# Kernel optimization log

Hardware: AMD Instinct MI355X
Metric: run time of the kernel (lower is better)

The kernel has to match this reference:

```python
import jax, jax.numpy as jnp
import numpy as np

D_MODEL = 1024
N_HEAD = 16


def setup_inputs() -> dict:
    key = jax.random.key(0)
    kx, kw = jax.random.split(key)
    x = jax.random.normal(kx, (4, 2048, D_MODEL), dtype=jnp.float32)
    # fused QKV projection weight, torch Linear: y = x @ W.T, W: [3*d_model, d_model]
    W_qkv = jax.random.normal(kw, (3 * D_MODEL, D_MODEL), dtype=jnp.float32) * (D_MODEL ** -0.5)
    return {"x": x, "W_qkv": W_qkv}


def reference(x, W_qkv):
    B, T, C = x.shape
    hd = C // N_HEAD
    qkv = jnp.einsum('btc,fc->btf', x, W_qkv)  # [B,T,3C]
    q, k, v = jnp.split(qkv, 3, axis=-1)
    # [B, H, T, hd]
    q = q.reshape(B, T, N_HEAD, hd).transpose(0, 2, 1, 3)
    k = k.reshape(B, T, N_HEAD, hd).transpose(0, 2, 1, 3)
    v = v.reshape(B, T, N_HEAD, hd).transpose(0, 2, 1, 3)
    scale = 1.0 / jnp.sqrt(jnp.asarray(hd, dtype=x.dtype))
    scores = jnp.einsum('bhqd,bhkd->bhqk', q, k) * scale  # [B,H,T,T]
    causal = jnp.tril(jnp.ones((T, T), dtype=bool))
    scores = jnp.where(causal, scores, jnp.asarray(-jnp.inf, dtype=scores.dtype))
    w = jax.nn.softmax(scores, axis=-1)
    out = jnp.einsum('bhqk,bhkd->bhqd', w, v)  # [B,H,T,hd]
    return out
```

## Files before the change

### kernel.cpp

```cpp
#include <hip/hip_runtime.h>
#include <hip/hip_bf16.h>
#include <math.h>

#define D_MODEL 1024
#define N_HEAD  16
#define HD      64
#define B_SZ    4
#define T_SEQ   2048
#define M_TOT   (B_SZ * T_SEQ)
#define N_TOT   (3 * D_MODEL)

typedef __bf16 bf16_t;
typedef __bf16 bf16x8 __attribute__((ext_vector_type(8)));
typedef __bf16 bf16x4 __attribute__((ext_vector_type(4)));
typedef __bf16 bf16x2 __attribute__((ext_vector_type(2)));
typedef float  f32x4  __attribute__((ext_vector_type(4)));
typedef float  f32x16 __attribute__((ext_vector_type(16)));
typedef int    i32x4  __attribute__((ext_vector_type(4)));

#define Q_PRESCALE 0.18033688011112042f

__device__ inline float fexp2(float x) { return __builtin_amdgcn_exp2f(x); }

__global__ __launch_bounds__(256) void cvt_f32_bf16(const float* __restrict__ in,
                                                    bf16_t* __restrict__ out, int n4) {
  int i = blockIdx.x * blockDim.x + threadIdx.x;
  int stride = gridDim.x * blockDim.x;
  for (; i < n4; i += stride) {
    float4 v = ((const float4*)in)[i];
    bf16x4 o;
    o[0] = (bf16_t)v.x; o[1] = (bf16_t)v.y; o[2] = (bf16_t)v.z; o[3] = (bf16_t)v.w;
    ((bf16x4*)out)[i] = o;
  }
}

__global__ __launch_bounds__(256) void qkv_gemm(const bf16_t* __restrict__ xb,
                                                const bf16_t* __restrict__ wb,
                                                bf16_t* __restrict__ Q,
                                                bf16_t* __restrict__ Kf,
                                                bf16_t* __restrict__ Vf) {
  __shared__ alignas(16) bf16_t smem[24576];
  bf16_t* a_lds = smem;
  bf16_t* b_lds = smem + 12288;
  bf16_t* c_lds = smem;

  const int tid  = threadIdx.x;
  const int wave = tid >> 6;
  const int lane = tid & 63;
  const int bm = blockIdx.y * 128;
  const int bn = blockIdx.x * 128;
  const int sec = bn >> 10;

  f32x4 acc[4][4] = {};

  const int sRow  = lane >> 2;
  const int sCol8 = (lane & 3) ^ ((lane >> 3) & 3);
  const int fr = lane & 15;
  const int fk = lane >> 4;
  const int wm = (wave >> 1) * 64;
  const int wn = (wave & 1) * 64;

  auto stage = [&](int buf, int kk) {
#pragma unroll
    for (int c = 0; c < 2; ++c) {
      const int chunk = wave * 2 + c;
      const bf16_t* gA = &xb[(size_t)(bm + chunk * 16 + sRow) * D_MODEL + kk + sCol8 * 8];
      __builtin_amdgcn_global_load_lds(
          (__attribute__((address_space(1))) void*)(void*)gA,
          (__attribute__((address_space(3))) void*)&a_lds[buf * 4096 + chunk * 512], 16, 0, 0);
      const bf16_t* gB = &wb[(size_t)(bn + chunk * 16 + sRow) * D_MODEL + kk + sCol8 * 8];
      __builtin_amdgcn_global_load_lds(
          (__attribute__((address_space(1))) void*)(void*)gB,
          (__attribute__((address_space(3))) void*)&b_lds[buf * 4096 + chunk * 512], 16, 0, 0);
    }
  };

  auto loadFrags = [&](int buf, bf16x8 af[4], bf16x8 bfr[4]) {
#pragma unroll
    for (int mt = 0; mt < 4; ++mt) {
      const int row = wm + mt * 16 + fr;
      af[mt] = *(const bf16x8*)&a_lds[buf * 4096 + row * 32 + (fk ^ ((fr >> 1) & 3)) * 8];
    }
#pragma unroll
    for (int nt = 0; nt < 4; ++nt) {
      const int row = wn + nt * 16 + fr;
      bfr[nt] = *(const bf16x8*)&b_lds[buf * 4096 + row * 32 + (fk ^ ((fr >> 1) & 3)) * 8];
    }
  };

  auto mfmaAll = [&](bf16x8 af[4], bf16x8 bfr[4]) {
    __builtin_amdgcn_s_setprio(1);
#pragma unroll
    for (int mt = 0; mt < 4; ++mt)
#pragma unroll
      for (int nt = 0; nt < 4; ++nt)
        acc[mt][nt] = __builtin_amdgcn_mfma_f32_16x16x32_bf16(af[mt], bfr[nt], acc[mt][nt], 0, 0, 0);
    __builtin_amdgcn_s_setprio(0);
  };

  stage(0, 0);
  stage(1, 32);
  int cur = 0;
  for (int t = 0; t < 31; ++t) {
    asm volatile("s_waitcnt vmcnt(4)" ::: "memory");
    __builtin_amdgcn_s_barrier();
    __builtin_amdgcn_sched_barrier(0);
    bf16x8 af[4], bfr[4];
    loadFrags(cur, af, bfr);
    if (t < 30) stage((t + 2) % 3, (t + 2) * 32);
    mfmaAll(af, bfr);
    cur = (cur + 1) % 3;
  }
  asm volatile("s_waitcnt vmcnt(0)" ::: "memory");
  __builtin_amdgcn_s_barrier();
  __builtin_amdgcn_sched_barrier(0);
  {
    bf16x8 af[4], bfr[4];
    loadFrags(cur, af, bfr);
    mfmaAll(af, bfr);
  }

  const int cRowBase = (lane >> 4) * 4;
  const int cCol     = lane & 15;

  if (sec == 2) {
#pragma unroll
    for (int mt = 0; mt < 4; ++mt) {
#pragma unroll
      for (int nt = 0; nt < 4; ++nt) {
        const int hn = (bn & 1023) + wn + nt * 16 + cCol;
        const int h  = hn >> 6;
        const int d  = hn & 63;
        const int mbase = bm + wm + mt * 16 + cRowBase;
        const int b  = mbase >> 11;
        const int t0 = mbase & 2047;
        const int kvt = t0 >> 5, tt0 = t0 & 31;
        const int idx = (d >> 5) * 2 + (tt0 >> 4);
        const int h2  = (tt0 >> 3) & 1;
        const int j0  = tt0 & 7;
        bf16x4 pk;
        pk[0] = (bf16_t)acc[mt][nt][0]; pk[1] = (bf16_t)acc[mt][nt][1];
        pk[2] = (bf16_t)acc[mt][nt][2]; pk[3] = (bf16_t)acc[mt][nt][3];
        const size_t bhOff = (size_t)(b * N_HEAD + h) * (T_SEQ * HD);
        *(bf16x4*)&Vf[bhOff + (size_t)(((kvt * 4 + idx) * 64 + h2 * 32 + (d & 31)) * 8 + j0)] = pk;
      }
    }
  } else {
    __syncthreads();
    const float qs = (sec == 0) ? Q_PRESCALE : 1.0f;
#pragma unroll
    for (int mt = 0; mt < 4; ++mt)
#pragma unroll
      for (int nt = 0; nt < 4; ++nt)
#pragma unroll
        for (int r = 0; r < 4; ++r) {
          const int mloc = wm + mt * 16 + cRowBase + r;
          const int nloc = wn + nt * 16 + cCol;
          c_lds[mloc * 132 + nloc] = (bf16_t)(acc[mt][nt][r] * qs);
        }
    __syncthreads();

    const int row = tid >> 1;
    const int nh  = tid & 1;
    const int m = bm + row;
    const int b = m >> 11, t = m & 2047;
    const int h = ((bn & 1023) + nh * 64) >> 6;
    const size_t bhOff = (size_t)(b * N_HEAD + h) * (T_SEQ * HD);

    if (sec == 0) {
      bf16_t* qp = Q + bhOff + (size_t)t * HD;
#pragma unroll
      for (int o = 0; o < 16; ++o) {
        bf16x4 vv = *(const bf16x4*)&c_lds[row * 132 + nh * 64 + o * 4];
        *(bf16x4*)&qp[o * 4] = vv;
      }
    } else {
      const int kvt = t >> 5, lk = t & 31;
#pragma unroll
      for (int o = 0; o < 16; ++o) {
        const int d0 = o * 4;
        const int cc = d0 >> 4, h2 = (d0 >> 3) & 1, j0 = d0 & 7;
        bf16x4 vv = *(const bf16x4*)&c_lds[row * 132 + nh * 64 + d0];
        *(bf16x4*)&Kf[bhOff + (size_t)(((kvt * 4 + cc) * 64 + h2 * 32 + lk) * 8 + j0)] = vv;
      }
    }
  }
}

__device__ inline int pack_bf16(float lo, float hi) {
  bf16x2 v; v[0] = (bf16_t)lo; v[1] = (bf16_t)hi;
  return __builtin_bit_cast(int, v);
}
__device__ inline void permswap(int& a, int& b) {
  asm volatile("v_permlane32_swap_b32 %0, %1" : "+v"(a), "+v"(b));
}

__global__ __launch_bounds__(256, 4) void attn_fwd(const bf16_t* __restrict__ Q,
                                                   const bf16_t* __restrict__ Kf,
                                                   const bf16_t* __restrict__ Vf,
                                                   float* __restrict__ out) {
  __shared__ float o_sh[2][64][33];
  __shared__ float m_sh[2][32];
  __shared__ float l_sh[2][32];

  const int tid  = threadIdx.x;
  const int wave = tid >> 6;
  const int lane = tid & 63;
  const int l31  = lane & 31;
  const int hi   = lane >> 5;

  const int f   = blockIdx.x;
  const int bh  = ((f & 7) << 3) | ((f >> 3) & 7);
  const int pr  = f >> 6;
  const int grp = wave >> 1;
  const int isWriter = wave & 1;
  const int chunk = grp ? (63 - pr) : pr;
  const int q0 = chunk * 32;
  const int n  = chunk + 1;
  const int h  = (n + 1) >> 1;
  const int j0 = isWriter ? h : 0;
  const int j1 = isWriter ? n : h;

  const bf16_t* Qp = Q  + (size_t)bh * T_SEQ * HD;
  const bf16_t* Kp = Kf + (size_t)bh * T_SEQ * HD;
  const bf16_t* Vp = Vf + (size_t)bh * T_SEQ * HD;
  float* op = out + (size_t)bh * T_SEQ * HD;

  bf16x8 qf[4];
#pragma unroll
  for (int c = 0; c < 4; ++c)
    qf[c] = *(const bf16x8*)&Qp[(size_t)(q0 + l31) * HD + c * 16 + hi * 8];

  f32x16 o0 = {}, o1 = {};
  float m_run = -INFINITY;
  float l_run = 0.f;

  if (j0 < j1) {
    const bf16_t* kp = Kp + (size_t)j0 * 2048 + lane * 8;
    const bf16_t* vp = Vp + (size_t)j0 * 2048 + lane * 8;
    bf16x8 kA[4], vA[4];
#pragma unroll
    for (int c = 0; c < 4; ++c) kA[c] = *(const bf16x8*)(kp + c * 512);
    kp += 2048;

    for (int j = j0; j < j1; ++j) {
      const int kv0 = j * 32;
#pragma unroll
      for (int idx = 0; idx < 4; ++idx) vA[idx] = *(const bf16x8*)(vp + idx * 512);
      vp += 2048;

      f32x16 st = {};
      __builtin_amdgcn_s_setprio(1);
#pragma unroll
      for (int c = 0; c < 4; ++c)
        st = __builtin_amdgcn_mfma_f32_32x32x16_bf16(kA[c], qf[c], st, 0, 0, 0);
      __builtin_amdgcn_s_setprio(0);

      if (j + 1 < j1) {
#pragma unroll
        for (int c = 0; c < 4; ++c) kA[c] = *(const bf16x8*)(kp + c * 512);
        kp += 2048;
      }

      if (kv0 == q0) {
#pragma unroll
        for (int r = 0; r < 16; ++r) {
          const int koff = (r & 3) + 8 * (r >> 2) + 4 * hi;
          st[r] = (koff > l31) ? -INFINITY : st[r];
        }
      }
      const float t0 = fmaxf(fmaxf(st[0],  st[1]),  st[2]);
      const float t1 = fmaxf(fmaxf(st[3],  st[4]),  st[5]);
      const float t2 = fmaxf(fmaxf(st[6],  st[7]),  st[8]);
      const float t3 = fmaxf(fmaxf(st[9],  st[10]), st[11]);
      const float t4 = fmaxf(fmaxf(st[12], st[13]), st[14]);
      float pm = fmaxf(fmaxf(fmaxf(t0, t1), t2), fmaxf(fmaxf(t3, t4), st[15]));

      if (__any(!(pm <= m_run + 8.f))) {
        const float pm_full = fmaxf(pm, __shfl_xor(pm, 32));
        const float m_new = fmaxf(m_run, pm_full);
        const float alpha = fexp2(m_run - m_new);
        m_run = m_new;
        l_run *= alpha;
#pragma unroll
        for (int r = 0; r < 16; ++r) {
          const int qr = (r & 3) + 8 * (r >> 2) + 4 * hi;
          const float av = __shfl(alpha, qr);
          o0[r] *= av; o1[r] *= av;
        }
      }

      float p[16];
#pragma unroll
      for (int r = 0; r < 16; ++r) p[r] = fexp2(st[r] - m_run);
      float s0 = (p[0] + p[1]) + (p[2] + p[3]);
      float s1 = (p[4] + p[5]) + (p[6] + p[7]);
      float s2 = (p[8] + p[9]) + (p[10] + p[11]);
      float s3 = (p[12] + p[13]) + (p[14] + p[15]);
      l_run += (s0 + s1) + (s2 + s3);

      int a01 = pack_bf16(p[0],  p[1]),  a23 = pack_bf16(p[2],  p[3]);
      int b01 = pack_bf16(p[4],  p[5]),  b23 = pack_bf16(p[6],  p[7]);
      int c01 = pack_bf16(p[8],  p[9]),  c23 = pack_bf16(p[10], p[11]);
      int d01 = pack_bf16(p[12], p[13]), d23 = pack_bf16(p[14], p[15]);
      permswap(a01, b01); permswap(a23, b23);
      permswap(c01, d01); permswap(c23, d23);
      i32x4 w1 = {a01, a23, b01, b23};
      i32x4 w2 = {c01, c23, d01, d23};
      bf16x8 f1 = __builtin_bit_cast(bf16x8, w1);
      bf16x8 f2 = __builtin_bit_cast(bf16x8, w2);

      __builtin_amdgcn_s_setprio(1);
      o0 = __builtin_amdgcn_mfma_f32_32x32x16_bf16(f1, vA[0], o0, 0, 0, 0);
      o0 = __builtin_amdgcn_mfma_f32_32x32x16_bf16(f2, vA[1], o0, 0, 0, 0);
      o1 = __builtin_amdgcn_mfma_f32_32x32x16_bf16(f1, vA[2], o1, 0, 0, 0);
      o1 = __builtin_amdgcn_mfma_f32_32x32x16_bf16(f2, vA[3], o1, 0, 0, 0);
      __builtin_amdgcn_s_setprio(0);
    }
  }

  const float l_comb = l_run + __shfl_xor(l_run, 32);

  if (isWriter) {
#pragma unroll
    for (int r = 0; r < 16; ++r) {
      o_sh[grp][lane][r]      = o0[r];
      o_sh[grp][lane][16 + r] = o1[r];
    }
    if (lane < 32) {
      m_sh[grp][lane] = m_run;
      l_sh[grp][lane] = l_comb;
    }
  }
  __syncthreads();
  if (!isWriter) {
#pragma unroll
    for (int r = 0; r < 16; ++r) {
      const int qr = (r & 3) + 8 * (r >> 2) + 4 * hi;
      const float mB = m_sh[grp][qr];
      const float lB = l_sh[grp][qr];
      const float mA = __shfl(m_run, qr);
      const float lA = __shfl(l_comb, qr);
      const float mM = fmaxf(mA, mB);
      const float aA = fexp2(mA - mM);
      const float aB = fexp2(mB - mM);
      const float li = 1.f / (lA * aA + lB * aB);
      const float x0 = (o0[r] * aA + o_sh[grp][lane][r]      * aB) * li;
      const float x1 = (o1[r] * aA + o_sh[grp][lane][16 + r] * aB) * li;
      op[(size_t)(q0 + qr) * HD + l31]      = x0;
      op[(size_t)(q0 + qr) * HD + 32 + l31] = x1;
    }
  }
}

extern "C" void kernel_launch(void* const* d_in, const int* in_sizes, int n_in,
                              void* d_out, int out_size, void* d_ws, size_t ws_size,
                              hipStream_t stream) {
  const float* x = (const float*)d_in[0];
  const float* W = (const float*)d_in[1];
  float* out = (float*)d_out;

  char* ws = (char*)d_ws;
  bf16_t* xb  = (bf16_t*)(ws);
  bf16_t* wb  = (bf16_t*)(ws + 16777216);
  bf16_t* Qb  = (bf16_t*)(ws + 16777216 + 6291456);
  bf16_t* Kfb = Qb + 8388608;
  bf16_t* Vfb = Kfb + 8388608;

  cvt_f32_bf16<<<2048, 256, 0, stream>>>(x, xb, (M_TOT * D_MODEL) / 4);
  cvt_f32_bf16<<<1024, 256, 0, stream>>>(W, wb, (N_TOT * D_MODEL) / 4);

  dim3 ggrid(N_TOT / 128, M_TOT / 128);
  qkv_gemm<<<ggrid, 256, 0, stream>>>(xb, wb, Qb, Kfb, Vfb);

  attn_fwd<<<2048, 256, 0, stream>>>(Qb, Kfb, Vfb, out);
}
```

Before: 137.7 us.

## Enlarge QKV GEMM tile to 256x128 with 8 waves and fuse conversions

The QKV projection GEMM now uses 512-thread blocks covering 256 rows by 128 columns, so each W tile staged in LDS is reused by twice as many rows, with a two-pass epilogue through LDS. The two f32-to-bf16 conversion launches are merged into one kernel to remove a launch. The larger tile raises LDS use and halves the number of blocks, which may reduce occupancy or tail balance. The vmcnt wait count and the store mapping are adjusted to match the new staging layout.

```diff
diff --git a/kernel.cpp b/kernel.cpp
--- a/kernel.cpp
+++ b/kernel.cpp
@@ -22,32 +22,37 @@
 
 __device__ inline float fexp2(float x) { return __builtin_amdgcn_exp2f(x); }
 
-__global__ __launch_bounds__(256) void cvt_f32_bf16(const float* __restrict__ in,
-                                                    bf16_t* __restrict__ out, int n4) {
+__global__ __launch_bounds__(256) void cvt_both(const float* __restrict__ x,
+                                                bf16_t* __restrict__ xb, int n4x,
+                                                const float* __restrict__ W,
+                                                bf16_t* __restrict__ wb, int n4w) {
   int i = blockIdx.x * blockDim.x + threadIdx.x;
   int stride = gridDim.x * blockDim.x;
-  for (; i < n4; i += stride) {
-    float4 v = ((const float4*)in)[i];
+  const int ntot = n4x + n4w;
+  for (; i < ntot; i += stride) {
+    const float4* src = (i < n4x) ? &((const float4*)x)[i] : &((const float4*)W)[i - n4x];
+    bf16x4* dst = (i < n4x) ? &((bf16x4*)xb)[i] : &((bf16x4*)wb)[i - n4x];
+    float4 v = *src;
     bf16x4 o;
     o[0] = (bf16_t)v.x; o[1] = (bf16_t)v.y; o[2] = (bf16_t)v.z; o[3] = (bf16_t)v.w;
-    ((bf16x4*)out)[i] = o;
-  }
-}
-
-__global__ __launch_bounds__(256) void qkv_gemm(const bf16_t* __restrict__ xb,
+    *dst = o;
+  }
+}
+
+__global__ __launch_bounds__(512) void qkv_gemm(const bf16_t* __restrict__ xb,
                                                 const bf16_t* __restrict__ wb,
                                                 bf16_t* __restrict__ Q,
                                                 bf16_t* __restrict__ Kf,
                                                 bf16_t* __restrict__ Vf) {
-  __shared__ alignas(16) bf16_t smem[24576];
+  __shared__ alignas(16) bf16_t smem[36864];
   bf16_t* a_lds = smem;
-  bf16_t* b_lds = smem + 12288;
+  bf16_t* b_lds = smem + 24576;
   bf16_t* c_lds = smem;
 
   const int tid  = threadIdx.x;
   const int wave = tid >> 6;
   const int lane = tid & 63;
-  const int bm = blockIdx.y * 128;
+  const int bm = blockIdx.y * 256;
   const int bn = blockIdx.x * 128;
   const int sec = bn >> 10;
 
@@ -67,7 +72,10 @@
       const bf16_t* gA = &xb[(size_t)(bm + chunk * 16 + sRow) * D_MODEL + kk + sCol8 * 8];
       __builtin_amdgcn_global_load_lds(
           (__attribute__((address_space(1))) void*)(void*)gA,
-          (__attribute__((address_space(3))) void*)&a_lds[buf * 4096 + chunk * 512], 16, 0, 0);
+          (__attribute__((address_space(3))) void*)&a_lds[buf * 8192 + chunk * 512], 16, 0, 0);
+    }
+    {
+      const int chunk = wave;
       const bf16_t* gB = &wb[(size_t)(bn + chunk * 16 + sRow) * D_MODEL + kk + sCol8 * 8];
       __builtin_amdgcn_global_load_lds(
           (__attribute__((address_space(1))) void*)(void*)gB,
@@ -79,7 +87,7 @@
 #pragma unroll
     for (int mt = 0; mt < 4; ++mt) {
       const int row = wm + mt * 16 + fr;
-      af[mt] = *(const bf16x8*)&a_lds[buf * 4096 + row * 32 + (fk ^ ((fr >> 1) & 3)) * 8];
+      af[mt] = *(const bf16x8*)&a_lds[buf * 8192 + row * 32 + (fk ^ ((fr >> 1) & 3)) * 8];
     }
 #pragma unroll
     for (int nt = 0; nt < 4; ++nt) {
@@ -102,7 +110,7 @@
   stage(1, 32);
   int cur = 0;
   for (int t = 0; t < 31; ++t) {
-    asm volatile("s_waitcnt vmcnt(4)" ::: "memory");
+    asm volatile("s_waitcnt vmcnt(3)" ::: "memory");
     __builtin_amdgcn_s_barrier();
     __builtin_amdgcn_sched_barrier(0);
     bf16x8 af[4], bfr[4];
@@ -146,43 +154,51 @@
       }
     }
   } else {
+    const float qs = (sec == 0) ? Q_PRESCALE : 1.0f;
     __syncthreads();
-    const float qs = (sec == 0) ? Q_PRESCALE : 1.0f;
-#pragma unroll
-    for (int mt = 0; mt < 4; ++mt)
-#pragma unroll
-      for (int nt = 0; nt < 4; ++nt)
-#pragma unroll
-        for (int r = 0; r < 4; ++r) {
-          const int mloc = wm + mt * 16 + cRowBase + r;
-          const int nloc = wn + nt * 16 + cCol;
-          c_lds[mloc * 132 + nloc] = (bf16_t)(acc[mt][nt][r] * qs);
+#pragma unroll
+    for (int pass = 0; pass < 2; ++pass) {
+      if ((wave >> 2) == pass) {
+#pragma unroll
+        for (int mt = 0; mt < 4; ++mt)
+#pragma unroll
+          for (int nt = 0; nt < 4; ++nt)
+#pragma unroll
+            for (int r = 0; r < 4; ++r) {
+              const int mloc = wm - pass * 128 + mt * 16 + cRowBase + r;
+              const int nloc = wn + nt * 16 + cCol;
+              c_lds[mloc * 132 + nloc] = (bf16_t)(acc[mt][nt][r] * qs);
+            }
+      }
+      __syncthreads();
+
+      const int row = tid >> 2;
+      const int cg  = tid & 3;
+      const int m = bm + pass * 128 + row;
+      const int b = m >> 11, t = m & 2047;
+      const size_t bhBase = (size_t)(b * N_HEAD) * (T_SEQ * HD);
+      if (sec == 0) {
+#pragma unroll
+        for (int o = 0; o < 8; ++o) {
+          const int col = cg * 32 + o * 4;
+          const int hn = (bn & 1023) + col;
+          bf16x4 vv = *(const bf16x4*)&c_lds[row * 132 + col];
+          *(bf16x4*)&Q[bhBase + (size_t)(hn >> 6) * (T_SEQ * HD) + (size_t)t * HD + (hn & 63)] = vv;
         }
-    __syncthreads();
-
-    const int row = tid >> 1;
-    const int nh  = tid & 1;
-    const int m = bm + row;
-    const int b = m >> 11, t = m & 2047;
-    const int h = ((bn & 1023) + nh * 64) >> 6;
-    const size_t bhOff = (size_t)(b * N_HEAD + h) * (T_SEQ * HD);
-
-    if (sec == 0) {
-      bf16_t* qp = Q + bhOff + (size_t)t * HD;
-#pragma unroll
-      for (int o = 0; o < 16; ++o) {
-        bf16x4 vv = *(const bf16x4*)&c_lds[row * 132 + nh * 64 + o * 4];
-        *(bf16x4*)&qp[o * 4] = vv;
-      }
-    } else {
-      const int kvt = t >> 5, lk = t & 31;
-#pragma unroll
-      for (int o = 0; o < 16; ++o) {
-        const int d0 = o * 4;
-        const int cc = d0 >> 4, h2 = (d0 >> 3) & 1, j0 = d0 & 7;
-        bf16x4 vv = *(const bf16x4*)&c_lds[row * 132 + nh * 64 + d0];
-        *(bf16x4*)&Kf[bhOff + (size_t)(((kvt * 4 + cc) * 64 + h2 * 32 + lk) * 8 + j0)] = vv;
-      }
+      } else {
+        const int kvt = t >> 5, lk = t & 31;
+#pragma unroll
+        for (int o = 0; o < 8; ++o) {
+          const int col = cg * 32 + o * 4;
+          const int hn = (bn & 1023) + col;
+          const int d0 = hn & 63;
+          const int cc = d0 >> 4, h2 = (d0 >> 3) & 1, j0 = d0 & 7;
+          bf16x4 vv = *(const bf16x4*)&c_lds[row * 132 + col];
+          *(bf16x4*)&Kf[bhBase + (size_t)(hn >> 6) * (T_SEQ * HD) +
+                        (size_t)(((kvt * 4 + cc) * 64 + h2 * 32 + lk) * 8 + j0)] = vv;
+        }
+      }
+      __syncthreads();
     }
   }
 }
@@ -367,11 +383,11 @@
   bf16_t* Kfb = Qb + 8388608;
   bf16_t* Vfb = Kfb + 8388608;
 
-  cvt_f32_bf16<<<2048, 256, 0, stream>>>(x, xb, (M_TOT * D_MODEL) / 4);
-  cvt_f32_bf16<<<1024, 256, 0, stream>>>(W, wb, (N_TOT * D_MODEL) / 4);
-
-  dim3 ggrid(N_TOT / 128, M_TOT / 128);
-  qkv_gemm<<<ggrid, 256, 0, stream>>>(xb, wb, Qb, Kfb, Vfb);
+  cvt_both<<<2048, 256, 0, stream>>>(x, xb, (M_TOT * D_MODEL) / 4,
+                                     W, wb, (N_TOT * D_MODEL) / 4);
+
+  dim3 ggrid(N_TOT / 128, M_TOT / 256);
+  qkv_gemm<<<ggrid, 512, 0, stream>>>(xb, wb, Qb, Kfb, Vfb);
 
   attn_fwd<<<2048, 256, 0, stream>>>(Qb, Kfb, Vfb, out);
 }
```

Result: no change. 139.3 us (+1.2%).
